# Performance work log

Hardware: AMD Instinct MI355X
Metric: run time of the kernel (lower is better)

## Reference

```python
import jax, jax.numpy as jnp
import numpy as np

D_IN, D_HID, D_OUT = 256, 256, 10  # mlp dims (init_kwargs)


def mlp(params, x):
    # x: [D_IN] (single sample, matching fnet_single's unsqueeze/squeeze)
    h = jnp.tanh(x @ params["W1"] + params["b1"])
    h = jnp.tanh(h @ params["W2"] + params["b2"])
    return h @ params["W3"] + params["b3"]  # [D_OUT]


def setup_inputs() -> dict:
    key = jax.random.key(0)
    ks = jax.random.split(key, 8)
    rn = lambda k, shp, scale: (jax.random.normal(k, shp, jnp.float32) * scale)
    return {
        "x1": jax.random.normal(ks[0], (64, D_IN), jnp.float32),
        "x2": jax.random.normal(ks[1], (64, D_IN), jnp.float32),
        "W1": rn(ks[2], (D_IN, D_HID), 1.0 / np.sqrt(D_IN)),
        "b1": jnp.zeros((D_HID,), jnp.float32),
        "W2": rn(ks[3], (D_HID, D_HID), 1.0 / np.sqrt(D_HID)),
        "b2": jnp.zeros((D_HID,), jnp.float32),
        "W3": rn(ks[4], (D_HID, D_OUT), 1.0 / np.sqrt(D_HID)),
        "b3": jnp.zeros((D_OUT,), jnp.float32),
    }


def reference(x1, x2, W1, b1, W2, b2, W3, b3):
    params = {"W1": W1, "b1": b1, "W2": W2, "b2": b2, "W3": W3, "b3": b3}
    # vmap(jacrev(fnet_single), (None, 0)): per-sample Jacobian w.r.t. every param tensor
    jac_fn = jax.vmap(jax.jacrev(mlp, argnums=0), in_axes=(None, 0))
    jac1 = jax.tree_util.tree_leaves(jac_fn(params, x1))  # list of [N, O, *pshape]
    jac2 = jax.tree_util.tree_leaves(jac_fn(params, x2))  # list of [M, O, *pshape]
    # flatten(2): [N, O, f] per param tensor
    j1 = [j.reshape(j.shape[0], j.shape[1], -1) for j in jac1]
    j2 = [j.reshape(j.shape[0], j.shape[1], -1) for j in jac2]
    # per-param einsum, then sum over param tensors (== stack(...).sum(0))
    result = sum(jnp.einsum("Naf,Mbf->NMab", a, b) for a, b in zip(j1, j2))
    return result  # [N, M, O, O]
```

## Files before the change

kernel.cpp:

```cpp
#include <hip/hip_runtime.h>

#define NS 64
#define D  256
#define O  10
#define TK 32
#define LSTR 36

__global__ __launch_bounds__(512) void prep1_kernel(
    const float* __restrict__ x1, const float* __restrict__ x2,
    const float* __restrict__ W1, const float* __restrict__ b1,
    const float* __restrict__ W2, const float* __restrict__ b2,
    const float* __restrict__ W3,
    float* __restrict__ h1o, float* __restrict__ S1o,
    float* __restrict__ h2o, float* __restrict__ G2L,
    float* __restrict__ W2T)
{
    int t = threadIdx.x;
    if (blockIdx.x >= 128) {
        int blk = blockIdx.x - 128;
        int bxT = blk & 7, byT = blk >> 3;
        __shared__ float tile[32][33];
        int txT = t & 31, tyT = t >> 5;
        #pragma unroll
        for (int r = 0; r < 2; ++r)
            tile[tyT + 16 * r][txT] = W2[(byT * 32 + tyT + 16 * r) * D + bxT * 32 + txT];
        __syncthreads();
        #pragma unroll
        for (int r = 0; r < 2; ++r)
            W2T[(bxT * 32 + tyT + 16 * r) * D + byT * 32 + txT] = tile[txT][tyT + 16 * r];
        return;
    }

    int s = blockIdx.x;
    const float* x = (s < NS) ? (x1 + s * D) : (x2 + (s - NS) * D);
    int tt = t & 255, half = t >> 8;
    int k0 = half * 128;
    __shared__ float xs[D];
    __shared__ float hs[D];
    __shared__ float part[2][D];

    if (half == 0) xs[tt] = x[tt];
    __syncthreads();

    float acc = half ? 0.0f : b1[tt];
    #pragma unroll 8
    for (int k = 0; k < 128; ++k) acc = fmaf(xs[k0 + k], W1[(k0 + k) * D + tt], acc);
    part[half][tt] = acc;
    __syncthreads();

    if (half == 0) {
        float h1v = tanhf(part[0][tt] + part[1][tt]);
        h1o[s * D + tt] = h1v;
        S1o[s * D + tt] = 1.0f - h1v * h1v;
        hs[tt] = h1v;
    }
    __syncthreads();

    acc = half ? 0.0f : b2[tt];
    #pragma unroll 8
    for (int k = 0; k < 128; ++k) acc = fmaf(hs[k0 + k], W2[(k0 + k) * D + tt], acc);
    part[half][tt] = acc;
    __syncthreads();

    if (half == 0) {
        float h2v = tanhf(part[0][tt] + part[1][tt]);
        h2o[s * D + tt] = h2v;
        hs[tt] = 1.0f - h2v * h2v;
    }
    __syncthreads();

    for (int idx = t; idx < O * D; idx += 512) {
        int a = idx >> 8, i = idx & 255;
        G2L[(s * O + a) * D + i] = hs[i] * W3[i * O + a];
    }
}

__global__ __launch_bounds__(512) void prep2_kernel(
    const float* __restrict__ W2T, const float* __restrict__ S1,
    const float* __restrict__ G2L, float* __restrict__ G1L,
    const float* __restrict__ x1, const float* __restrict__ x2,
    const float* __restrict__ h1, const float* __restrict__ h2,
    float* __restrict__ dots)
{
    int t = threadIdx.x;
    if (blockIdx.x < 128) {
        int s = blockIdx.x;
        __shared__ float g2s[O * D];
        __shared__ float red[O * D];
        for (int idx = t; idx < D * O; idx += 512) g2s[idx] = G2L[s * D * O + idx];
        __syncthreads();

        int tt = t & 255, half = t >> 8;
        int j0 = half * 128;
        float acc[O];
        #pragma unroll
        for (int a = 0; a < O; ++a) acc[a] = 0.0f;
        #pragma unroll 8
        for (int j = 0; j < 128; ++j) {
            float w = W2T[(j0 + j) * D + tt];
            #pragma unroll
            for (int a = 0; a < O; ++a) acc[a] = fmaf(w, g2s[a * D + j0 + j], acc[a]);
        }
        if (half == 1) {
            #pragma unroll
            for (int a = 0; a < O; ++a) red[a * D + tt] = acc[a];
        }
        __syncthreads();
        if (half == 0) {
            float s1 = S1[s * D + tt];
            #pragma unroll
            for (int a = 0; a < O; ++a)
                G1L[(s * O + a) * D + tt] = s1 * (acc[a] + red[a * D + tt]);
        }
        return;
    }

    int idx = blockIdx.x - 128;
    int which = idx >> 6, n = idx & 63;
    const float* A; const float* B;
    if (which == 0)      { A = x1 + n * D; B = x2; }
    else if (which == 1) { A = h1 + n * D; B = h1 + NS * D; }
    else                 { A = h2 + n * D; B = h2 + NS * D; }
    __shared__ float as[D];
    if (t < D) as[t] = A[t];
    __syncthreads();
    int wave = t >> 6, lane = t & 63;
    for (int m = wave; m < NS; m += 8) {
        const float* Bv = B + m * D;
        float v = as[lane] * Bv[lane]
                + as[64 + lane] * Bv[64 + lane]
                + as[128 + lane] * Bv[128 + lane]
                + as[192 + lane] * Bv[192 + lane];
        #pragma unroll
        for (int off = 32; off > 0; off >>= 1) v += __shfl_xor(v, off);
        if (lane == 0) dots[(which * NS + n) * NS + m] = v;
    }
}

__global__ __launch_bounds__(256) void ntk_gemm_kernel(
    const float* __restrict__ G1L, const float* __restrict__ G2L,
    float* __restrict__ P1p, float* __restrict__ P2p)
{
    int tile = blockIdx.x % 100;
    int ks   = blockIdx.x / 100;
    int by = tile / 10, bx = tile % 10;
    __shared__ float A1[64 * LSTR], B1[64 * LSTR], A2[64 * LSTR], B2[64 * LSTR];
    int t = threadIdx.x;
    int tx = t & 15, ty = t >> 4;

    float acc1[4][4], acc2[4][4];
    #pragma unroll
    for (int i = 0; i < 4; ++i)
        #pragma unroll
        for (int j = 0; j < 4; ++j) { acc1[i][j] = 0.0f; acc2[i][j] = 0.0f; }

    const float* arow1 = G1L + (by * 64) * D + ks * 64;
    const float* brow1 = G1L + (640 + bx * 64) * D + ks * 64;
    const float* arow2 = G2L + (by * 64) * D + ks * 64;
    const float* brow2 = G2L + (640 + bx * 64) * D + ks * 64;

    for (int kc = 0; kc < 64; kc += TK) {
        __syncthreads();
        #pragma unroll
        for (int u = 0; u < 2; ++u) {
            int idx = t + u * 256;
            int r = idx >> 3, c4 = idx & 7;
            int goff = r * D + kc + c4 * 4;
            int loff = r * LSTR + c4 * 4;
            *(float4*)&A1[loff] = *(const float4*)&arow1[goff];
            *(float4*)&B1[loff] = *(const float4*)&brow1[goff];
            *(float4*)&A2[loff] = *(const float4*)&arow2[goff];
            *(float4*)&B2[loff] = *(const float4*)&brow2[goff];
        }
        __syncthreads();
        #pragma unroll
        for (int kk = 0; kk < TK; kk += 4) {
            float4 a1[4], b1v[4], a2[4], b2v[4];
            #pragma unroll
            for (int i = 0; i < 4; ++i) {
                a1[i] = *(const float4*)&A1[(4 * ty + i) * LSTR + kk];
                a2[i] = *(const float4*)&A2[(4 * ty + i) * LSTR + kk];
            }
            #pragma unroll
            for (int j = 0; j < 4; ++j) {
                b1v[j] = *(const float4*)&B1[(tx + 16 * j) * LSTR + kk];
                b2v[j] = *(const float4*)&B2[(tx + 16 * j) * LSTR + kk];
            }
            #pragma unroll
            for (int i = 0; i < 4; ++i)
                #pragma unroll
                for (int j = 0; j < 4; ++j) {
                    acc1[i][j] = fmaf(a1[i].x, b1v[j].x, acc1[i][j]);
                    acc1[i][j] = fmaf(a1[i].y, b1v[j].y, acc1[i][j]);
                    acc1[i][j] = fmaf(a1[i].z, b1v[j].z, acc1[i][j]);
                    acc1[i][j] = fmaf(a1[i].w, b1v[j].w, acc1[i][j]);
                    acc2[i][j] = fmaf(a2[i].x, b2v[j].x, acc2[i][j]);
                    acc2[i][j] = fmaf(a2[i].y, b2v[j].y, acc2[i][j]);
                    acc2[i][j] = fmaf(a2[i].z, b2v[j].z, acc2[i][j]);
                    acc2[i][j] = fmaf(a2[i].w, b2v[j].w, acc2[i][j]);
                }
        }
    }

    #pragma unroll
    for (int i = 0; i < 4; ++i) {
        int R = by * 64 + 4 * ty + i;
        float* p1row = P1p + (ks * 640 + R) * 640;
        float* p2row = P2p + (ks * 640 + R) * 640;
        #pragma unroll
        for (int j = 0; j < 4; ++j) {
            int C = bx * 64 + tx + 16 * j;
            p1row[C] = acc1[i][j];
            p2row[C] = acc2[i][j];
        }
    }
}

__global__ __launch_bounds__(256) void combine_kernel(
    const float* __restrict__ P1p, const float* __restrict__ P2p,
    const float* __restrict__ dots, float* __restrict__ out)
{
    int base = blockIdx.x * 1024;
    #pragma unroll
    for (int u = 0; u < 4; ++u) {
        int e = base + u * 256 + threadIdx.x;
        int R = e / 640, C = e - R * 640;
        float p1 = 0.0f, p2 = 0.0f;
        #pragma unroll
        for (int s = 0; s < 4; ++s) {
            p1 += P1p[(s * 640 + R) * 640 + C];
            p2 += P2p[(s * 640 + R) * 640 + C];
        }
        int n = R / 10, a = R - n * 10;
        int m = C / 10, b = C - m * 10;
        float cx  = 1.0f + dots[0 * NS * NS + n * NS + m];
        float ch1 = 1.0f + dots[1 * NS * NS + n * NS + m];
        float val = cx * p1 + ch1 * p2;
        if (a == b) val += 1.0f + dots[2 * NS * NS + n * NS + m];
        out[(n * NS + m) * (O * O) + a * O + b] = val;
    }
}

extern "C" void kernel_launch(void* const* d_in, const int* in_sizes, int n_in,
                              void* d_out, int out_size, void* d_ws, size_t ws_size,
                              hipStream_t stream) {
    const float* x1 = (const float*)d_in[0];
    const float* x2 = (const float*)d_in[1];
    const float* W1 = (const float*)d_in[2];
    const float* b1 = (const float*)d_in[3];
    const float* W2 = (const float*)d_in[4];
    const float* b2 = (const float*)d_in[5];
    const float* W3 = (const float*)d_in[6];

    float* ws   = (float*)d_ws;
    float* h1   = ws;
    float* S1   = h1 + 128 * D;
    float* h2   = S1 + 128 * D;
    float* G2L  = h2 + 128 * D;
    float* G1L  = G2L + 1280 * D;
    float* W2T  = G1L + 1280 * D;
    float* dots = W2T + D * D;
    float* P1p  = dots + 3 * NS * NS;
    float* P2p  = P1p + 4 * 640 * 640;
    float* out  = (float*)d_out;

    hipLaunchKernelGGL(prep1_kernel, dim3(192), dim3(512), 0, stream,
                       x1, x2, W1, b1, W2, b2, W3, h1, S1, h2, G2L, W2T);
    hipLaunchKernelGGL(prep2_kernel, dim3(320), dim3(512), 0, stream,
                       W2T, S1, G2L, G1L, x1, x2, h1, h2, dots);
    hipLaunchKernelGGL(ntk_gemm_kernel, dim3(400), dim3(256), 0, stream,
                       G1L, G2L, P1p, P2p);
    hipLaunchKernelGGL(combine_kernel, dim3(400), dim3(256), 0, stream,
                       P1p, P2p, dots, out);
}
```

Measured before the change: 115.8 us.

## Fuse split-K combine into GEMM epilogue with atomics and zero output early

Removes the combine kernel and the split-K partial buffers. The GEMM epilogue now applies the dot-product scaling and atomically adds into the output, which extra blocks in the first kernel zero beforehand. The GEMM loads its full 64-wide K slice in one shared-memory stage, and the W2T reduction in prep2 reads g2s as float4. This saves one launch and the round trip through the partial buffers, at the cost of atomic contention (4 adds per output element) and a nondeterministic summation order.

```diff
diff --git a/kernel.cpp b/kernel.cpp
--- a/kernel.cpp
+++ b/kernel.cpp
@@ -3,8 +3,8 @@
 #define NS 64
 #define D  256
 #define O  10
-#define TK 32
-#define LSTR 36
+#define TK 64
+#define LSTR 68
 
 __global__ __launch_bounds__(512) void prep1_kernel(
     const float* __restrict__ x1, const float* __restrict__ x2,
@@ -13,9 +13,19 @@
     const float* __restrict__ W3,
     float* __restrict__ h1o, float* __restrict__ S1o,
     float* __restrict__ h2o, float* __restrict__ G2L,
-    float* __restrict__ W2T)
+    float* __restrict__ W2T, float* __restrict__ out)
 {
     int t = threadIdx.x;
+    if (blockIdx.x >= 192) {
+        int idx = (blockIdx.x - 192) * 512 + t;
+        float4* o4 = (float4*)out;
+        #pragma unroll
+        for (int u = 0; u < 4; ++u) {
+            int e = idx + u * 32768;
+            if (e < 102400) o4[e] = make_float4(0.f, 0.f, 0.f, 0.f);
+        }
+        return;
+    }
     if (blockIdx.x >= 128) {
         int blk = blockIdx.x - 128;
         int bxT = blk & 7, byT = blk >> 3;
@@ -95,11 +105,20 @@
         float acc[O];
         #pragma unroll
         for (int a = 0; a < O; ++a) acc[a] = 0.0f;
-        #pragma unroll 8
-        for (int j = 0; j < 128; ++j) {
-            float w = W2T[(j0 + j) * D + tt];
-            #pragma unroll
-            for (int a = 0; a < O; ++a) acc[a] = fmaf(w, g2s[a * D + j0 + j], acc[a]);
+        #pragma unroll 2
+        for (int j = 0; j < 128; j += 4) {
+            float w0 = W2T[(j0 + j + 0) * D + tt];
+            float w1 = W2T[(j0 + j + 1) * D + tt];
+            float w2 = W2T[(j0 + j + 2) * D + tt];
+            float w3 = W2T[(j0 + j + 3) * D + tt];
+            #pragma unroll
+            for (int a = 0; a < O; ++a) {
+                float4 g = *(const float4*)&g2s[a * D + j0 + j];
+                acc[a] = fmaf(w0, g.x, acc[a]);
+                acc[a] = fmaf(w1, g.y, acc[a]);
+                acc[a] = fmaf(w2, g.z, acc[a]);
+                acc[a] = fmaf(w3, g.w, acc[a]);
+            }
         }
         if (half == 1) {
             #pragma unroll
@@ -139,7 +158,7 @@
 
 __global__ __launch_bounds__(256) void ntk_gemm_kernel(
     const float* __restrict__ G1L, const float* __restrict__ G2L,
-    float* __restrict__ P1p, float* __restrict__ P2p)
+    const float* __restrict__ dots, float* __restrict__ out)
 {
     int tile = blockIdx.x % 100;
     int ks   = blockIdx.x / 100;
@@ -159,85 +178,61 @@
     const float* arow2 = G2L + (by * 64) * D + ks * 64;
     const float* brow2 = G2L + (640 + bx * 64) * D + ks * 64;
 
-    for (int kc = 0; kc < 64; kc += TK) {
-        __syncthreads();
-        #pragma unroll
-        for (int u = 0; u < 2; ++u) {
-            int idx = t + u * 256;
-            int r = idx >> 3, c4 = idx & 7;
-            int goff = r * D + kc + c4 * 4;
-            int loff = r * LSTR + c4 * 4;
-            *(float4*)&A1[loff] = *(const float4*)&arow1[goff];
-            *(float4*)&B1[loff] = *(const float4*)&brow1[goff];
-            *(float4*)&A2[loff] = *(const float4*)&arow2[goff];
-            *(float4*)&B2[loff] = *(const float4*)&brow2[goff];
-        }
-        __syncthreads();
-        #pragma unroll
-        for (int kk = 0; kk < TK; kk += 4) {
-            float4 a1[4], b1v[4], a2[4], b2v[4];
-            #pragma unroll
-            for (int i = 0; i < 4; ++i) {
-                a1[i] = *(const float4*)&A1[(4 * ty + i) * LSTR + kk];
-                a2[i] = *(const float4*)&A2[(4 * ty + i) * LSTR + kk];
+    #pragma unroll
+    for (int u = 0; u < 4; ++u) {
+        int idx = t + u * 256;
+        int r = idx >> 4, c4 = idx & 15;
+        int goff = r * D + c4 * 4;
+        int loff = r * LSTR + c4 * 4;
+        *(float4*)&A1[loff] = *(const float4*)&arow1[goff];
+        *(float4*)&B1[loff] = *(const float4*)&brow1[goff];
+        *(float4*)&A2[loff] = *(const float4*)&arow2[goff];
+        *(float4*)&B2[loff] = *(const float4*)&brow2[goff];
+    }
+    __syncthreads();
+
+    #pragma unroll
+    for (int kk = 0; kk < TK; kk += 4) {
+        float4 a1[4], b1v[4], a2[4], b2v[4];
+        #pragma unroll
+        for (int i = 0; i < 4; ++i) {
+            a1[i] = *(const float4*)&A1[(4 * ty + i) * LSTR + kk];
+            a2[i] = *(const float4*)&A2[(4 * ty + i) * LSTR + kk];
+        }
+        #pragma unroll
+        for (int j = 0; j < 4; ++j) {
+            b1v[j] = *(const float4*)&B1[(tx + 16 * j) * LSTR + kk];
+            b2v[j] = *(const float4*)&B2[(tx + 16 * j) * LSTR + kk];
+        }
+        #pragma unroll
+        for (int i = 0; i < 4; ++i)
+            #pragma unroll
+            for (int j = 0; j < 4; ++j) {
+                acc1[i][j] = fmaf(a1[i].x, b1v[j].x, acc1[i][j]);
+                acc1[i][j] = fmaf(a1[i].y, b1v[j].y, acc1[i][j]);
+                acc1[i][j] = fmaf(a1[i].z, b1v[j].z, acc1[i][j]);
+                acc1[i][j] = fmaf(a1[i].w, b1v[j].w, acc1[i][j]);
+                acc2[i][j] = fmaf(a2[i].x, b2v[j].x, acc2[i][j]);
+                acc2[i][j] = fmaf(a2[i].y, b2v[j].y, acc2[i][j]);
+                acc2[i][j] = fmaf(a2[i].z, b2v[j].z, acc2[i][j]);
+                acc2[i][j] = fmaf(a2[i].w, b2v[j].w, acc2[i][j]);
             }
-            #pragma unroll
-            for (int j = 0; j < 4; ++j) {
-                b1v[j] = *(const float4*)&B1[(tx + 16 * j) * LSTR + kk];
-                b2v[j] = *(const float4*)&B2[(tx + 16 * j) * LSTR + kk];
-            }
-            #pragma unroll
-            for (int i = 0; i < 4; ++i)
-                #pragma unroll
-                for (int j = 0; j < 4; ++j) {
-                    acc1[i][j] = fmaf(a1[i].x, b1v[j].x, acc1[i][j]);
-                    acc1[i][j] = fmaf(a1[i].y, b1v[j].y, acc1[i][j]);
-                    acc1[i][j] = fmaf(a1[i].z, b1v[j].z, acc1[i][j]);
-                    acc1[i][j] = fmaf(a1[i].w, b1v[j].w, acc1[i][j]);
-                    acc2[i][j] = fmaf(a2[i].x, b2v[j].x, acc2[i][j]);
-                    acc2[i][j] = fmaf(a2[i].y, b2v[j].y, acc2[i][j]);
-                    acc2[i][j] = fmaf(a2[i].z, b2v[j].z, acc2[i][j]);
-                    acc2[i][j] = fmaf(a2[i].w, b2v[j].w, acc2[i][j]);
-                }
-        }
     }
 
     #pragma unroll
     for (int i = 0; i < 4; ++i) {
         int R = by * 64 + 4 * ty + i;
-        float* p1row = P1p + (ks * 640 + R) * 640;
-        float* p2row = P2p + (ks * 640 + R) * 640;
+        int n = R / 10, a = R - n * 10;
         #pragma unroll
         for (int j = 0; j < 4; ++j) {
             int C = bx * 64 + tx + 16 * j;
-            p1row[C] = acc1[i][j];
-            p2row[C] = acc2[i][j];
-        }
-    }
-}
-
-__global__ __launch_bounds__(256) void combine_kernel(
-    const float* __restrict__ P1p, const float* __restrict__ P2p,
-    const float* __restrict__ dots, float* __restrict__ out)
-{
-    int base = blockIdx.x * 1024;
-    #pragma unroll
-    for (int u = 0; u < 4; ++u) {
-        int e = base + u * 256 + threadIdx.x;
-        int R = e / 640, C = e - R * 640;
-        float p1 = 0.0f, p2 = 0.0f;
-        #pragma unroll
-        for (int s = 0; s < 4; ++s) {
-            p1 += P1p[(s * 640 + R) * 640 + C];
-            p2 += P2p[(s * 640 + R) * 640 + C];
-        }
-        int n = R / 10, a = R - n * 10;
-        int m = C / 10, b = C - m * 10;
-        float cx  = 1.0f + dots[0 * NS * NS + n * NS + m];
-        float ch1 = 1.0f + dots[1 * NS * NS + n * NS + m];
-        float val = cx * p1 + ch1 * p2;
-        if (a == b) val += 1.0f + dots[2 * NS * NS + n * NS + m];
-        out[(n * NS + m) * (O * O) + a * O + b] = val;
+            int m = C / 10, b = C - m * 10;
+            float cx  = 1.0f + dots[0 * NS * NS + n * NS + m];
+            float ch1 = 1.0f + dots[1 * NS * NS + n * NS + m];
+            float val = cx * acc1[i][j] + ch1 * acc2[i][j];
+            if (ks == 0 && a == b) val += 1.0f + dots[2 * NS * NS + n * NS + m];
+            atomicAdd(&out[(n * NS + m) * (O * O) + a * O + b], val);
+        }
     }
 }
 
@@ -260,16 +255,12 @@
     float* G1L  = G2L + 1280 * D;
     float* W2T  = G1L + 1280 * D;
     float* dots = W2T + D * D;
-    float* P1p  = dots + 3 * NS * NS;
-    float* P2p  = P1p + 4 * 640 * 640;
     float* out  = (float*)d_out;
 
-    hipLaunchKernelGGL(prep1_kernel, dim3(192), dim3(512), 0, stream,
-                       x1, x2, W1, b1, W2, b2, W3, h1, S1, h2, G2L, W2T);
+    hipLaunchKernelGGL(prep1_kernel, dim3(256), dim3(512), 0, stream,
+                       x1, x2, W1, b1, W2, b2, W3, h1, S1, h2, G2L, W2T, out);
     hipLaunchKernelGGL(prep2_kernel, dim3(320), dim3(512), 0, stream,
                        W2T, S1, G2L, G1L, x1, x2, h1, h2, dots);
     hipLaunchKernelGGL(ntk_gemm_kernel, dim3(400), dim3(256), 0, stream,
-                       G1L, G2L, P1p, P2p);
-    hipLaunchKernelGGL(combine_kernel, dim3(400), dim3(256), 0, stream,
-                       P1p, P2p, dots, out);
-}
+                       G1L, G2L, dots, out);
+}
```

New measurement: 353.4 us. +205.1%, slower.
